# Kernel optimization log

Measured on AMD Instinct MI355X. Metric: run time of the kernel, lower is better.

Reference implementation:

```python
import jax, jax.numpy as jnp
import numpy as np

H = 16      # num_head
DH = 64     # d_head
D = H * DH  # d_model
NEG = -10000.0


def _proj(x, W, b):
    # torch Linear: y = x @ W^T + b
    return jnp.einsum('bld,od->blo', x, W) + b


def _heads(x):
    b, l, _ = x.shape
    return x.reshape(b, l, H, DH)


def _attn_logits(feat_q, mask_q, feat_k, mask_k, Wq, bq, Wk, bk):
    q = _heads(_proj(feat_q, Wq, bq))   # b lq h dh
    k = _heads(_proj(feat_k, Wk, bk))   # b lk h dh
    logits = jnp.einsum('bqhd,bkhd->bhqk', q, k)
    m = mask_q[:, None, :, None] & mask_k[:, None, None, :]  # b 1 lq lk
    return jnp.where(m, logits, NEG)


def setup_inputs() -> dict:
    key = jax.random.key(0)
    ks = jax.random.split(key, 12)
    B, Lv, Lt = 4, 1024, 256
    scale = 1.0 / np.sqrt(D).astype(np.float32)
    inp = {
        'vid_feat': jax.random.normal(ks[0], (B, Lv, D), jnp.float32),
        'vid_mask': jax.random.bernoulli(ks[1], 0.9, (B, Lv)),
        'txt_feat': jax.random.normal(ks[2], (B, Lt, D), jnp.float32),
        'txt_mask': jax.random.bernoulli(ks[3], 0.9, (B, Lt)),
    }
    names = ['v2v', 't2v', 'v2t', 't2t']
    for i, n in enumerate(names):
        inp['W_' + n] = jax.random.normal(ks[4 + i], (3, D, D), jnp.float32) * scale
        inp['b_' + n] = jax.random.normal(ks[8 + i], (3, D), jnp.float32) * 0.01
    return inp


def reference(vid_feat, vid_mask, txt_feat, txt_mask,
              W_v2v, b_v2v, W_t2v, b_t2v, W_v2t, b_v2t, W_t2t, b_t2t):
    B, Lv, _ = vid_feat.shape
    B, Lt, _ = txt_feat.shape
    # sr_ratio == 1: vid_feat_sr == vid_feat, vid_mask_sr == vid_mask
    vid_feat_sr, vid_mask_sr = vid_feat, vid_mask

    # values (proj index 2), concatenated along key length
    v_value = jnp.concatenate([_proj(vid_feat_sr, W_v2v[2], b_v2v[2]),
                               _proj(txt_feat, W_t2v[2], b_t2v[2])], axis=1)
    v_value = _heads(v_value)  # b (Lv+Lt) h dh
    t_value = jnp.concatenate([_proj(vid_feat_sr, W_v2t[2], b_v2t[2]),
                               _proj(txt_feat, W_t2t[2], b_t2t[2])], axis=1)
    t_value = _heads(t_value)

    v2v = _attn_logits(vid_feat, vid_mask, vid_feat_sr, vid_mask_sr,
                       W_v2v[0], b_v2v[0], W_v2v[1], b_v2v[1])
    t2v = _attn_logits(vid_feat, vid_mask, txt_feat, txt_mask,
                       W_t2v[0], b_t2v[0], W_t2v[1], b_t2v[1])
    v2t = _attn_logits(txt_feat, txt_mask, vid_feat_sr, vid_mask_sr,
                       W_v2t[0], b_v2t[0], W_v2t[1], b_v2t[1])
    t2t = _attn_logits(txt_feat, txt_mask, txt_feat, txt_mask,
                       W_t2t[0], b_t2t[0], W_t2t[1], b_t2t[1])

    v_logits = jnp.concatenate([v2v, t2v], axis=-1)  # b h Lv (Lv+Lt)
    t_logits = jnp.concatenate([v2t, t2t], axis=-1)  # b h Lt (Lv+Lt)
    inv_sqrt_dh = jnp.float32(1.0 / np.sqrt(DH))

    # NOTE: original applies softmax, THEN divides by sqrt(d_head) (faithful)
    vid_out = jnp.einsum('bhqk,bkhd->bqhd',
                         jax.nn.softmax(v_logits, axis=-1) * inv_sqrt_dh,
                         v_value).reshape(B, Lv, D)
    txt_out = jnp.einsum('bhqk,bkhd->bqhd',
                         jax.nn.softmax(t_logits, axis=-1) * inv_sqrt_dh,
                         t_value).reshape(B, Lt, D)
    return vid_out, txt_out
```

## Files before the change

### kernel.cpp

```cpp
#include <hip/hip_runtime.h>


typedef __attribute__((ext_vector_type(8))) _Float16  half8;
typedef __attribute__((ext_vector_type(4))) _Float16  half4;
typedef __attribute__((ext_vector_type(4))) float     f32x4;
typedef __attribute__((ext_vector_type(4))) unsigned int uint4v;
typedef __attribute__((ext_vector_type(2))) unsigned int uint2v;

#define MFMA_F16   __builtin_amdgcn_mfma_f32_16x16x32_f16
#define MFMA16_F16 __builtin_amdgcn_mfma_f32_16x16x16f16

#define LOG2E 1.4426950408889634f
#define NEGB  (-14426.950408889634f)

static __device__ __forceinline__ unsigned short f_to_f16u(float f) {
  _Float16 h = (_Float16)f;
  return __builtin_bit_cast(unsigned short, h);
}

#define GLOAD_LDS16(g, l)                                            \
  __builtin_amdgcn_global_load_lds(                                  \
      (const __attribute__((address_space(1))) void*)(g),            \
      (__attribute__((address_space(3))) void*)(l), 16, 0, 0)

struct CvtDesc { const float* src; unsigned short* dst; int n8; };
struct CvtArgs { CvtDesc d[14]; };

__global__ __launch_bounds__(256) void cvt_fp16(CvtArgs ca) {
  const CvtDesc dd = ca.d[blockIdx.y];
  const int n16 = dd.n8 >> 1;
  const int stride = gridDim.x * blockDim.x;
  for (int i = blockIdx.x * blockDim.x + threadIdx.x; i < n16; i += stride) {
    const f32x4* src = (const f32x4*)dd.src + (size_t)i * 4;
    const f32x4 a = src[0];
    const f32x4 b = src[1];
    const f32x4 c = src[2];
    const f32x4 d = src[3];
    half8 h0, h1;
    h0[0] = (_Float16)a[0]; h0[1] = (_Float16)a[1];
    h0[2] = (_Float16)a[2]; h0[3] = (_Float16)a[3];
    h0[4] = (_Float16)b[0]; h0[5] = (_Float16)b[1];
    h0[6] = (_Float16)b[2]; h0[7] = (_Float16)b[3];
    h1[0] = (_Float16)c[0]; h1[1] = (_Float16)c[1];
    h1[2] = (_Float16)c[2]; h1[3] = (_Float16)c[3];
    h1[4] = (_Float16)d[0]; h1[5] = (_Float16)d[1];
    h1[6] = (_Float16)d[2]; h1[7] = (_Float16)d[3];
    half8* dst = (half8*)dd.dst + (size_t)i * 2;
    dst[0] = h0;
    dst[1] = h1;
  }
}

static __device__ __forceinline__ void copy_out_tile(
    const unsigned short* Cs, unsigned short* dst, int tid,
    int b, int l0, int h0, int Ld, int soff, int mode) {
  for (int i = 0; i < 8; ++i) {
    const int c     = i * 256 + tid;
    const int major = c >> 4;
    const int kc    = c & 15;
    if (mode == 1) {
      const int base = (kc >> 2) * 32 + (kc & 3) * 4;
      const int sw   = major & 7;
      const int o1   = major * 128 + (((base >> 3) ^ sw) << 3) + (base & 7);
      const int b2   = base + 16;
      const int o2   = major * 128 + (((b2 >> 3) ^ sw) << 3) + (b2 & 7);
      const uint2v lo = *(const uint2v*)&Cs[o1];
      const uint2v hi = *(const uint2v*)&Cs[o2];
      uint4v val; val[0] = lo[0]; val[1] = lo[1]; val[2] = hi[0]; val[3] = hi[1];
      const int hh = h0 + (major >> 6);
      const int dh = major & 63;
      const int k  = soff + l0 + (kc >> 2) * 32;
      const size_t el = (size_t)(b * 16 + hh) * 81920 + (size_t)(k >> 5) * 2048 +
                        dh * 32 + (kc & 3) * 8;
      *(uint4v*)(dst + el) = val;
    } else {
      const uint4v val =
          *(const uint4v*)&Cs[major * 128 + ((kc ^ (major & 7)) << 3)];
      if (mode == 0) {
        const size_t el =
            ((size_t)(b * 16 + h0 + (kc >> 3)) * Ld + soff + l0 + major) * 64 +
            (kc & 7) * 8;
        *(uint4v*)(dst + el) = val;
      } else {
        const int k   = soff + l0 + major;
        const int dh0 = (kc & 7) * 8;
        const size_t el = (size_t)(b * 16 + h0 + (kc >> 3)) * 81920 +
                          (size_t)(k >> 4) * 1024 + (dh0 >> 5) * 512 +
                          (k & 15) * 32 + ((dh0 >> 3) & 3) * 8;
        *(uint4v*)(dst + el) = val;
      }
    }
  }
}

struct ProjDescH {
  const unsigned short* X;
  const unsigned short* W;
  const float* Bv;
  unsigned short* dst;
  int M, lxsh, Ld, soff, mode;
  float oscale;
};
struct ProjArgsH { ProjDescH d[12]; };

__global__ __launch_bounds__(256) void proj_gemm_h(ProjArgsH pa) {
  const ProjDescH dd = pa.d[blockIdx.z];
  const int m0 = blockIdx.y * 128;
  if (m0 >= dd.M) return;
  const int n0 = blockIdx.x * 128;

  __shared__ __align__(16) unsigned char smem[32768];
  unsigned short* As = (unsigned short*)smem;
  unsigned short* Bs = As + 4096;
  unsigned short* Cs = (unsigned short*)smem;

  const int tid  = threadIdx.x;
  const int lane = tid & 63;
  const int w    = tid >> 6;
  const int wr   = (w >> 1) * 64;
  const int wc   = (w & 1) * 64;
  const int ql   = lane & 15;
  const int qd   = lane >> 4;

  f32x4 acc[4][4];
  for (int i = 0; i < 4; ++i)
    for (int j = 0; j < 4; ++j) acc[i][j] = (f32x4)(0.0f);

  const unsigned short* Xg = dd.X + (size_t)m0 * 1024;
  const unsigned short* Wg = dd.W + (size_t)n0 * 1024;

  for (int k0 = 0; k0 < 1024; k0 += 32) {
    __syncthreads();
    for (int half = 0; half < 2; ++half) {
      const int cb  = w * 128 + half * 64;
      const int c   = cb + lane;
      const int row = c >> 2;
      const int kcg = (c & 3) ^ (row & 3);
      GLOAD_LDS16(Xg + row * 1024 + k0 + kcg * 8, As + cb * 8);
      GLOAD_LDS16(Wg + row * 1024 + k0 + kcg * 8, Bs + cb * 8);
    }
    __syncthreads();

    half8 af[4], bf[4];
    for (int mt = 0; mt < 4; ++mt) {
      const int row = wr + mt * 16 + ql;
      af[mt] = *(const half8*)&As[row * 32 + ((qd ^ (row & 3)) << 3)];
    }
    for (int nt = 0; nt < 4; ++nt) {
      const int row = wc + nt * 16 + ql;
      bf[nt] = *(const half8*)&Bs[row * 32 + ((qd ^ (row & 3)) << 3)];
    }
    for (int mt = 0; mt < 4; ++mt)
      for (int nt = 0; nt < 4; ++nt)
        acc[mt][nt] = MFMA_F16(af[mt], bf[nt], acc[mt][nt], 0, 0, 0);
  }

  float bv[4];
  for (int nt = 0; nt < 4; ++nt)
    bv[nt] = dd.Bv[n0 + wc + nt * 16 + ql];

  __syncthreads();

  for (int mt = 0; mt < 4; ++mt) {
    for (int nt = 0; nt < 4; ++nt) {
      const int nl = wc + nt * 16 + ql;
      for (int r = 0; r < 4; ++r) {
        const int ml = wr + mt * 16 + qd * 4 + r;
        const int row = dd.mode == 1 ? nl : ml;
        const int col = dd.mode == 1 ? ml : nl;
        const float v = (acc[mt][nt][r] + bv[nt]) * dd.oscale;
        Cs[row * 128 + (((col >> 3) ^ (row & 7)) << 3) + (col & 7)] = f_to_f16u(v);
      }
    }
  }
  __syncthreads();

  copy_out_tile(Cs, dd.dst, tid, m0 >> dd.lxsh, m0 & ((1 << dd.lxsh) - 1),
                n0 >> 6, dd.Ld, dd.soff, dd.mode);
}

struct ProjDesc {
  const float* X;
  const float* W;
  const float* Bv;
  unsigned short* dst;
  int M, lxsh, Ld, soff, mode;
  float oscale;
};
struct ProjArgs { ProjDesc d[12]; };

static __device__ __forceinline__ half8 cvt8sw(const float* base, int row, int g0) {
  const int sw = row & 7;
  const f32x4 a = *(const f32x4*)(base + (row * 8 + (g0 ^ sw)) * 4);
  const f32x4 b = *(const f32x4*)(base + (row * 8 + ((g0 + 1) ^ sw)) * 4);
  half8 h;
  h[0] = (_Float16)a[0]; h[1] = (_Float16)a[1];
  h[2] = (_Float16)a[2]; h[3] = (_Float16)a[3];
  h[4] = (_Float16)b[0]; h[5] = (_Float16)b[1];
  h[6] = (_Float16)b[2]; h[7] = (_Float16)b[3];
  return h;
}

__global__ __launch_bounds__(256) void proj_gemm_f32(ProjArgs pa) {
  const ProjDesc dd = pa.d[blockIdx.z];
  const int m0 = blockIdx.y * 128;
  if (m0 >= dd.M) return;
  const int n0 = blockIdx.x * 128;

  __shared__ __align__(16) unsigned char smem[32768];
  float* As = (float*)smem;
  float* Bs = As + 4096;
  unsigned short* Cs = (unsigned short*)smem;

  const int tid  = threadIdx.x;
  const int lane = tid & 63;
  const int w    = tid >> 6;
  const int wr   = (w >> 1) * 64;
  const int wc   = (w & 1) * 64;
  const int ql   = lane & 15;
  const int qd   = lane >> 4;

  f32x4 acc[4][4];
  for (int i = 0; i < 4; ++i)
    for (int j = 0; j < 4; ++j) acc[i][j] = (f32x4)(0.0f);

  const float* Xg = dd.X + (size_t)m0 * 1024;
  const float* Wg = dd.W + (size_t)n0 * 1024;

  for (int k0 = 0; k0 < 1024; k0 += 32) {
    __syncthreads();
    for (int j = 0; j < 4; ++j) {
      const int cb  = (j * 4 + w) * 64;
      const int c   = cb + lane;
      const int row = c >> 3;
      const int kcg = (c & 7) ^ (row & 7);
      GLOAD_LDS16(Xg + row * 1024 + k0 + kcg * 4, As + cb * 4);
      GLOAD_LDS16(Wg + row * 1024 + k0 + kcg * 4, Bs + cb * 4);
    }
    __syncthreads();

    half8 af[4], bf[4];
    for (int mt = 0; mt < 4; ++mt)
      af[mt] = cvt8sw(As, wr + mt * 16 + ql, qd * 2);
    for (int nt = 0; nt < 4; ++nt)
      bf[nt] = cvt8sw(Bs, wc + nt * 16 + ql, qd * 2);
    for (int mt = 0; mt < 4; ++mt)
      for (int nt = 0; nt < 4; ++nt)
        acc[mt][nt] = MFMA_F16(af[mt], bf[nt], acc[mt][nt], 0, 0, 0);
  }

  float bv[4];
  for (int nt = 0; nt < 4; ++nt)
    bv[nt] = dd.Bv[n0 + wc + nt * 16 + ql];

  __syncthreads();

  for (int mt = 0; mt < 4; ++mt) {
    for (int nt = 0; nt < 4; ++nt) {
      const int nl = wc + nt * 16 + ql;
      for (int r = 0; r < 4; ++r) {
        const int ml = wr + mt * 16 + qd * 4 + r;
        const int row = dd.mode == 1 ? nl : ml;
        const int col = dd.mode == 1 ? ml : nl;
        const float v = (acc[mt][nt][r] + bv[nt]) * dd.oscale;
        Cs[row * 128 + (((col >> 3) ^ (row & 7)) << 3) + (col & 7)] = f_to_f16u(v);
      }
    }
  }
  __syncthreads();

  copy_out_tile(Cs, dd.dst, tid, m0 >> dd.lxsh, m0 & ((1 << dd.lxsh) - 1),
                n0 >> 6, dd.Ld, dd.soff, dd.mode);
}

__global__ __launch_bounds__(256) void attn_flash7(
    const unsigned short* __restrict__ Qa_v, const unsigned short* __restrict__ Qb_v,
    const unsigned short* __restrict__ K_v,  const unsigned short* __restrict__ V_vT,
    const unsigned short* __restrict__ Qa_t, const unsigned short* __restrict__ Qb_t,
    const unsigned short* __restrict__ K_t,  const unsigned short* __restrict__ V_tT,
    const int* __restrict__ vmask, const int* __restrict__ tmask,
    float* __restrict__ out_v, float* __restrict__ out_t) {
  __shared__ __align__(16) unsigned short KVs[8192];
  __shared__ __align__(16) float kb_s[1280];

  const int bid = blockIdx.x;
  const int sid = (bid & 7) * 160 + (bid >> 3);
  const int bh  = sid / 20;
  const int sub = sid - bh * 20;

  const bool vside = sub < 16;
  const int  Lq    = vside ? 1024 : 256;
  const int  qblk  = vside ? sub : sub - 16;
  const unsigned short* Qa = vside ? Qa_v : Qa_t;
  const unsigned short* Qb = vside ? Qb_v : Qb_t;
  const unsigned short* K  = vside ? K_v  : K_t;
  const unsigned short* VT = vside ? V_vT : V_tT;
  const int* mq  = vside ? vmask : tmask;
  float*     out = vside ? out_v : out_t;

  const int b = bh >> 4;
  const int h = bh & 15;
  const int tid  = threadIdx.x;
  const int w    = tid >> 6;
  const int lane = tid & 63;
  const int ql = lane & 15, qd = lane >> 4;
  const int q0 = qblk * 64 + w * 16;

  const unsigned short* Kb = K  + (size_t)bh * 81920;
  const unsigned short* Vb = VT + (size_t)bh * 81920;

  {
    const int* kmv = vmask + b * 1024;
    const int* kmt = tmask + b * 256;
    for (int i = tid; i < 1280; i += 256) {
      const int mk = (i < 1024) ? kmv[i] : kmt[i - 1024];
      kb_s[i] = mk ? 0.0f : NEGB;
    }
  }

  const int gsw  = (tid ^ ((tid >> 3) & 3)) * 8;
  const int wlds = w * 512;

#define STAGE6(nb, k0s)                                                     \
  do {                                                                      \
    const unsigned short* Kt_ = Kb + (size_t)((k0s) >> 4) * 1024;           \
    const unsigned short* Vt_ = Vb + (size_t)((k0s) >> 5) * 2048;           \
    unsigned short* Ld_ = KVs + (nb) * 4096 + wlds;                         \
    GLOAD_LDS16(Kt_ + gsw, Ld_);                                            \
    GLOAD_LDS16(Vt_ + gsw, Ld_ + 2048);                                     \
  } while (0)

  STAGE6(0, 0);

  const unsigned short* Qab = Qa + ((size_t)bh * Lq + q0) * 64;
  const unsigned short* Qbb = Qb + ((size_t)bh * Lq + q0) * 64;
  half8 aA[2], aB[2];
  for (int ks = 0; ks < 2; ++ks) {
    aA[ks] = *(const half8*)&Qab[ql * 64 + ks * 32 + qd * 8];
    aB[ks] = *(const half8*)&Qbb[ql * 64 + ks * 32 + qd * 8];
  }
  const int mqs = mq[b * Lq + q0 + ql];

  const int swc = (qd ^ ((ql >> 1) & 3)) * 8;

  float m = -1e30f, l = 0.0f;
  f32x4 o[4];
  for (int nt = 0; nt < 4; ++nt) o[nt] = (f32x4)(0.0f);

  int cur = 0;
#define TILE7(tt, QF)                                                       \
  {                                                                         \
    __syncthreads();                    \
    if ((tt) < 39) STAGE6(cur ^ 1, ((tt) + 1) * 32);                        \
    const unsigned short* Ls = KVs + cur * 4096;                            \
    half8 vv[4];                                                            \
    for (int nt = 0; nt < 4; ++nt)                                          \
      vv[nt] = *(const half8*)&Ls[2048 + (nt * 16 + ql) * 32 + swc];        \
    f32x4 sv[2];                                                            \
    for (int s = 0; s < 2; ++s) {                                           \
      f32x4 S = *(const f32x4*)&kb_s[(tt) * 32 + s * 16 + qd * 4];          \
      const unsigned short* Kt = Ls + s * 1024;                             \
      const half8 kf0 = *(const half8*)&Kt[ql * 32 + swc];                  \
      const half8 kf1 = *(const half8*)&Kt[512 + ql * 32 + swc];            \
      S = MFMA_F16(kf0, QF[0], S, 0, 0, 0);                                 \
      S = MFMA_F16(kf1, QF[1], S, 0, 0, 0);                                 \
      for (int r = 0; r < 4; ++r) sv[s][r] = mqs ? S[r] : NEGB;             \
    }                                                                       \
    const float t0 = fmaxf(fmaxf(sv[0][0], sv[0][1]), sv[0][2]);            \
    const float t1 = fmaxf(fmaxf(sv[0][3], sv[1][0]), sv[1][1]);            \
    const float t2 = fmaxf(fmaxf(sv[1][2], sv[1][3]), t0);                  \
    float bm = fmaxf(t1, t2);                                               \
    bm = fmaxf(bm, __shfl_xor(bm, 16, 64));                                 \
    bm = fmaxf(bm, __shfl_xor(bm, 32, 64));                                 \
    if (__any(bm > m)) {                        \
      const float nm = fmaxf(m, bm);                                        \
      const float alpha = __builtin_amdgcn_exp2f(m - nm);                   \
      l *= alpha;                                                           \
      for (int nt = 0; nt < 4; ++nt)                                        \
        for (int r = 0; r < 4; ++r) o[nt][r] *= alpha;                      \
      m = nm;                                                               \
    }                                                                       \
    half4 pv[2];                                                            \
    float lsum = 0.0f;                                                      \
    for (int s = 0; s < 2; ++s)                                             \
      for (int r = 0; r < 4; ++r) {                                         \
        const float p = __builtin_amdgcn_exp2f(sv[s][r] - m);               \
        lsum += p;                                                          \
        pv[s][r] = (_Float16)p;                                             \
      }                                                                     \
    l += lsum;                                                              \
    for (int nt = 0; nt < 4; ++nt) {                                        \
      const half4 vlo = __builtin_shufflevector(vv[nt], vv[nt], 0, 1, 2, 3);\
      const half4 vhi = __builtin_shufflevector(vv[nt], vv[nt], 4, 5, 6, 7);\
      o[nt] = MFMA16_F16(vlo, pv[0], o[nt], 0, 0, 0);                       \
      o[nt] = MFMA16_F16(vhi, pv[1], o[nt], 0, 0, 0);                       \
    }                                                                       \
    cur ^= 1;                                                               \
  }

  for (int t = 0; t < 32; ++t) TILE7(t, aA);
  for (int t = 32; t < 40; ++t) TILE7(t, aB);
#undef TILE7
#undef STAGE6

  l += __shfl_xor(l, 16, 64);
  l += __shfl_xor(l, 32, 64);
  const float inv = 0.125f / l;

  float* ob = out + ((size_t)(b * Lq + q0 + ql)) * 1024 + h * 64;
  for (int nt = 0; nt < 4; ++nt) {
    f32x4 r;
    for (int j = 0; j < 4; ++j) r[j] = o[nt][j] * inv;
    *(f32x4*)(ob + nt * 16 + qd * 4) = r;
  }
}

extern "C" void kernel_launch(void* const* d_in, const int* in_sizes, int n_in,
                              void* d_out, int out_size, void* d_ws, size_t ws_size,
                              hipStream_t stream) {
  const float* vid   = (const float*)d_in[0];
  const int*   vmask = (const int*)d_in[1];
  const float* txt   = (const float*)d_in[2];
  const int*   tmask = (const int*)d_in[3];
  const float* Wsrc[4] = {(const float*)d_in[4], (const float*)d_in[6],
                          (const float*)d_in[8], (const float*)d_in[10]};
  const float* Bsrc[4] = {(const float*)d_in[5], (const float*)d_in[7],
                          (const float*)d_in[9], (const float*)d_in[11]};

  const int DD = 1024 * 1024, Dm = 1024, MEG = 1048576;

  unsigned short* ws = (unsigned short*)d_ws;
  unsigned short* Qa_v = ws;
  unsigned short* Qb_v = ws + 4194304;
  unsigned short* K_v  = ws + 8388608;
  unsigned short* V_vT = ws + 13631488;
  unsigned short* Qa_t = ws + 18874368;
  unsigned short* Qb_t = ws + 19922944;
  unsigned short* K_t  = ws + 20971520;
  unsigned short* V_tT = ws + 26214400;
  unsigned short* Xv_h = ws + 31457280;
  unsigned short* Xt_h = ws + 35651584;
  unsigned short* Wh   = ws + 36700160;

  const size_t need = (size_t)49283072 * 2;
  const bool use_h = ws_size >= need;

  if (use_h) {
    CvtArgs ca;
    ca.d[0] = CvtDesc{vid, Xv_h, 4194304 / 8};
    ca.d[1] = CvtDesc{txt, Xt_h, 1048576 / 8};
    for (int s = 0; s < 4; ++s)
      for (int j = 0; j < 3; ++j)
        ca.d[2 + s * 3 + j] = CvtDesc{Wsrc[s] + j * DD, Wh + (s * 3 + j) * MEG, DD / 8};
    cvt_fp16<<<dim3(256, 14), dim3(256), 0, stream>>>(ca);

    ProjArgsH pa;
    auto set = [&](int i, const unsigned short* X, int wi, const float* Bv,
                   unsigned short* dst, int M, int lxsh, int Ld, int soff, int mode,
                   float osc) {
      pa.d[i] = ProjDescH{X, Wh + wi * MEG, Bv, dst, M, lxsh, Ld, soff, mode, osc};
    };
    set(0,  Xv_h, 0,  Bsrc[0],          Qa_v, 4096, 10, 1024, 0,    0, LOG2E);
    set(1,  Xv_h, 1,  Bsrc[0] + Dm,     K_v,  4096, 10, 1280, 0,    2, 1.0f);
    set(2,  Xv_h, 2,  Bsrc[0] + 2 * Dm, V_vT, 4096, 10, 1280, 0,    1, 1.0f);
    set(3,  Xv_h, 3,  Bsrc[1],          Qb_v, 4096, 10, 1024, 0,    0, LOG2E);
    set(4,  Xt_h, 4,  Bsrc[1] + Dm,     K_v,  1024, 8,  1280, 1024, 2, 1.0f);
    set(5,  Xt_h, 5,  Bsrc[1] + 2 * Dm, V_vT, 1024, 8,  1280, 1024, 1, 1.0f);
    set(6,  Xt_h, 6,  Bsrc[2],          Qa_t, 1024, 8,  256,  0,    0, LOG2E);
    set(7,  Xv_h, 7,  Bsrc[2] + Dm,     K_t,  4096, 10, 1280, 0,    2, 1.0f);
    set(8,  Xv_h, 8,  Bsrc[2] + 2 * Dm, V_tT, 4096, 10, 1280, 0,    1, 1.0f);
    set(9,  Xt_h, 9,  Bsrc[3],          Qb_t, 1024, 8,  256,  0,    0, LOG2E);
    set(10, Xt_h, 10, Bsrc[3] + Dm,     K_t,  1024, 8,  1280, 1024, 2, 1.0f);
    set(11, Xt_h, 11, Bsrc[3] + 2 * Dm, V_tT, 1024, 8,  1280, 1024, 1, 1.0f);

    proj_gemm_h<<<dim3(8, 32, 12), dim3(256), 0, stream>>>(pa);
  } else {
    ProjArgs pa;
    auto set = [&](int i, const float* X, const float* W, const float* Bv,
                   unsigned short* dst, int M, int lxsh, int Ld, int soff, int mode,
                   float osc) {
      pa.d[i] = ProjDesc{X, W, Bv, dst, M, lxsh, Ld, soff, mode, osc};
    };
    set(0,  vid, Wsrc[0],          Bsrc[0],          Qa_v, 4096, 10, 1024, 0,    0, LOG2E);
    set(1,  vid, Wsrc[0] + DD,     Bsrc[0] + Dm,     K_v,  4096, 10, 1280, 0,    2, 1.0f);
    set(2,  vid, Wsrc[0] + 2 * DD, Bsrc[0] + 2 * Dm, V_vT, 4096, 10, 1280, 0,    1, 1.0f);
    set(3,  vid, Wsrc[1],          Bsrc[1],          Qb_v, 4096, 10, 1024, 0,    0, LOG2E);
    set(4,  txt, Wsrc[1] + DD,     Bsrc[1] + Dm,     K_v,  1024, 8,  1280, 1024, 2, 1.0f);
    set(5,  txt, Wsrc[1] + 2 * DD, Bsrc[1] + 2 * Dm, V_vT, 1024, 8,  1280, 1024, 1, 1.0f);
    set(6,  txt, Wsrc[2],          Bsrc[2],          Qa_t, 1024, 8,  256,  0,    0, LOG2E);
    set(7,  vid, Wsrc[2] + DD,     Bsrc[2] + Dm,     K_t,  4096, 10, 1280, 0,    2, 1.0f);
    set(8,  vid, Wsrc[2] + 2 * DD, Bsrc[2] + 2 * Dm, V_tT, 4096, 10, 1280, 0,    1, 1.0f);
    set(9,  txt, Wsrc[3],          Bsrc[3],          Qb_t, 1024, 8,  256,  0,    0, LOG2E);
    set(10, txt, Wsrc[3] + DD,     Bsrc[3] + Dm,     K_t,  1024, 8,  1280, 1024, 2, 1.0f);
    set(11, txt, Wsrc[3] + 2 * DD, Bsrc[3] + 2 * Dm, V_tT, 1024, 8,  1280, 1024, 1, 1.0f);

    proj_gemm_f32<<<dim3(8, 32, 12), dim3(256), 0, stream>>>(pa);
  }

  float* out_v = (float*)d_out;
  float* out_t = out_v + 4 * 1024 * 1024;
  attn_flash7<<<dim3(1280), dim3(256), 0, stream>>>(
      Qa_v, Qb_v, K_v, V_vT, Qa_t, Qb_t, K_t, V_tT,
      vmask, tmask, out_v, out_t);
}
```

Measured before the change: 286.1 us.

## Double-buffer projection GEMM LDS tiles with async prefetch of next k-slice

The projection GEMM now uses two LDS buffers, each holding an A and a B tile. It issues the global-to-LDS loads for the next 32-wide k slice before computing on the current one, and waits with vmcnt(4) so that only the older loads must be complete. The goal is to hide global load latency behind the MFMA work instead of stalling on every iteration. This depends on the 32KB of shared memory fitting two buffers and on hand-placed waitcnt and barrier ordering being correct.

Measured after the change: 299.2 us. 1.05x slower.

```diff
diff --git a/kernel.cpp b/kernel.cpp
--- a/kernel.cpp
+++ b/kernel.cpp
@@ -110,8 +110,7 @@
   const int n0 = blockIdx.x * 128;
 
   __shared__ __align__(16) unsigned char smem[32768];
-  unsigned short* As = (unsigned short*)smem;
-  unsigned short* Bs = As + 4096;
+  unsigned short* AB = (unsigned short*)smem;
   unsigned short* Cs = (unsigned short*)smem;
 
   const int tid  = threadIdx.x;
@@ -129,18 +128,34 @@
   const unsigned short* Xg = dd.X + (size_t)m0 * 1024;
   const unsigned short* Wg = dd.W + (size_t)n0 * 1024;
 
-  for (int k0 = 0; k0 < 1024; k0 += 32) {
-    __syncthreads();
-    for (int half = 0; half < 2; ++half) {
-      const int cb  = w * 128 + half * 64;
-      const int c   = cb + lane;
-      const int row = c >> 2;
-      const int kcg = (c & 3) ^ (row & 3);
-      GLOAD_LDS16(Xg + row * 1024 + k0 + kcg * 8, As + cb * 8);
-      GLOAD_LDS16(Wg + row * 1024 + k0 + kcg * 8, Bs + cb * 8);
-    }
-    __syncthreads();
-
+#define STAGEP(nb, k0s)                                                      \
+  do {                                                                       \
+    unsigned short* As_ = AB + (nb) * 8192;                                  \
+    for (int half_ = 0; half_ < 2; ++half_) {                                \
+      const int cb_  = w * 128 + half_ * 64;                                 \
+      const int c_   = cb_ + lane;                                           \
+      const int row_ = c_ >> 2;                                              \
+      const int kcg_ = (c_ & 3) ^ (row_ & 3);                                \
+      GLOAD_LDS16(Xg + row_ * 1024 + (k0s) + kcg_ * 8, As_ + cb_ * 8);       \
+      GLOAD_LDS16(Wg + row_ * 1024 + (k0s) + kcg_ * 8, As_ + 4096 + cb_ * 8);\
+    }                                                                        \
+  } while (0)
+
+  STAGEP(0, 0);
+
+  for (int t = 0; t < 32; ++t) {
+    __builtin_amdgcn_s_barrier();
+    if (t < 31) {
+      STAGEP((t + 1) & 1, (t + 1) * 32);
+      asm volatile("s_waitcnt vmcnt(4)" ::: "memory");
+    } else {
+      asm volatile("s_waitcnt vmcnt(0)" ::: "memory");
+    }
+    __builtin_amdgcn_sched_barrier(0);
+    __builtin_amdgcn_s_barrier();
+
+    const unsigned short* As = AB + (t & 1) * 8192;
+    const unsigned short* Bs = As + 4096;
     half8 af[4], bf[4];
     for (int mt = 0; mt < 4; ++mt) {
       const int row = wr + mt * 16 + ql;
@@ -154,6 +169,7 @@
       for (int nt = 0; nt < 4; ++nt)
         acc[mt][nt] = MFMA_F16(af[mt], bf[nt], acc[mt][nt], 0, 0, 0);
   }
+#undef STAGEP
 
   float bv[4];
   for (int nt = 0; nt < 4; ++nt)
```

## Enlarge f16 projection GEMM tile to 256x128 with 512-thread blocks

Applied to the files above, without the earlier changes.

The half-precision projection GEMM now uses 512-thread blocks covering 256 rows by 128 columns, so each weight tile loaded into LDS is shared by twice as many rows and the grid is halved. The epilogue stages the two 128-row halves through shared memory one after the other, and copy_out_tile takes a thread count so it works with either block size. The change targets redundant weight loads and per-block overhead, at the cost of fewer blocks for the GPU to schedule and extra barriers in the epilogue.

After: 286.9 us. No clear change (+0.3%).

```diff
diff --git a/kernel.cpp b/kernel.cpp
--- a/kernel.cpp
+++ b/kernel.cpp
@@ -52,10 +52,9 @@
 }
 
 static __device__ __forceinline__ void copy_out_tile(
-    const unsigned short* Cs, unsigned short* dst, int tid,
+    const unsigned short* Cs, unsigned short* dst, int tid, int nthr,
     int b, int l0, int h0, int Ld, int soff, int mode) {
-  for (int i = 0; i < 8; ++i) {
-    const int c     = i * 256 + tid;
+  for (int c = tid; c < 2048; c += nthr) {
     const int major = c >> 4;
     const int kc    = c & 15;
     if (mode == 1) {
@@ -103,15 +102,124 @@
 };
 struct ProjArgsH { ProjDescH d[12]; };
 
-__global__ __launch_bounds__(256) void proj_gemm_h(ProjArgsH pa) {
+__global__ __launch_bounds__(512) void proj_gemm_h(ProjArgsH pa) {
   const ProjDescH dd = pa.d[blockIdx.z];
+  const int m0 = blockIdx.y * 256;
+  if (m0 >= dd.M) return;
+  const int n0 = blockIdx.x * 128;
+
+  __shared__ __align__(16) unsigned char smem[32768];
+  unsigned short* As = (unsigned short*)smem;
+  unsigned short* Bs = As + 8192;
+  unsigned short* Cs = (unsigned short*)smem;
+
+  const int tid  = threadIdx.x;
+  const int lane = tid & 63;
+  const int w    = tid >> 6;
+  const int wrF  = (w >> 1) * 64;
+  const int wc   = (w & 1) * 64;
+  const int ql   = lane & 15;
+  const int qd   = lane >> 4;
+
+  f32x4 acc[4][4];
+  for (int i = 0; i < 4; ++i)
+    for (int j = 0; j < 4; ++j) acc[i][j] = (f32x4)(0.0f);
+
+  const unsigned short* Xg = dd.X + (size_t)m0 * 1024;
+  const unsigned short* Wg = dd.W + (size_t)n0 * 1024;
+
+  for (int k0 = 0; k0 < 1024; k0 += 32) {
+    __syncthreads();
+    {
+      const int cb0 = w * 64;
+      const int c0  = cb0 + lane;
+      const int r0  = c0 >> 2;
+      GLOAD_LDS16(Xg + r0 * 1024 + k0 + ((c0 & 3) ^ (r0 & 3)) * 8, As + cb0 * 8);
+      const int cb1 = 512 + w * 64;
+      const int c1  = cb1 + lane;
+      const int r1  = c1 >> 2;
+      GLOAD_LDS16(Xg + r1 * 1024 + k0 + ((c1 & 3) ^ (r1 & 3)) * 8, As + cb1 * 8);
+      const int cb2 = w * 64;
+      const int c2  = cb2 + lane;
+      const int r2  = c2 >> 2;
+      GLOAD_LDS16(Wg + r2 * 1024 + k0 + ((c2 & 3) ^ (r2 & 3)) * 8, Bs + cb2 * 8);
+    }
+    __syncthreads();
+
+    half8 af[4], bf[4];
+    for (int mt = 0; mt < 4; ++mt) {
+      const int row = wrF + mt * 16 + ql;
+      af[mt] = *(const half8*)&As[row * 32 + ((qd ^ (row & 3)) << 3)];
+    }
+    for (int nt = 0; nt < 4; ++nt) {
+      const int row = wc + nt * 16 + ql;
+      bf[nt] = *(const half8*)&Bs[row * 32 + ((qd ^ (row & 3)) << 3)];
+    }
+    for (int mt = 0; mt < 4; ++mt)
+      for (int nt = 0; nt < 4; ++nt)
+        acc[mt][nt] = MFMA_F16(af[mt], bf[nt], acc[mt][nt], 0, 0, 0);
+  }
+
+  float bv[4];
+  for (int nt = 0; nt < 4; ++nt)
+    bv[nt] = dd.Bv[n0 + wc + nt * 16 + ql];
+
+  for (int rh = 0; rh < 2; ++rh) {
+    __syncthreads();
+    if ((w >> 2) == rh) {
+      const int wrL = ((w >> 1) & 1) * 64;
+      for (int mt = 0; mt < 4; ++mt) {
+        for (int nt = 0; nt < 4; ++nt) {
+          const int nl = wc + nt * 16 + ql;
+          for (int r = 0; r < 4; ++r) {
+            const int ml = wrL + mt * 16 + qd * 4 + r;
+            const int row = dd.mode == 1 ? nl : ml;
+            const int col = dd.mode == 1 ? ml : nl;
+            const float v = (acc[mt][nt][r] + bv[nt]) * dd.oscale;
+            Cs[row * 128 + (((col >> 3) ^ (row & 7)) << 3) + (col & 7)] =
+                f_to_f16u(v);
+          }
+        }
+      }
+    }
+    __syncthreads();
+    const int m0p = m0 + rh * 128;
+    copy_out_tile(Cs, dd.dst, tid, 512, m0p >> dd.lxsh,
+                  m0p & ((1 << dd.lxsh) - 1), n0 >> 6, dd.Ld, dd.soff, dd.mode);
+  }
+}
+
+struct ProjDesc {
+  const float* X;
+  const float* W;
+  const float* Bv;
+  unsigned short* dst;
+  int M, lxsh, Ld, soff, mode;
+  float oscale;
+};
+struct ProjArgs { ProjDesc d[12]; };
+
+static __device__ __forceinline__ half8 cvt8sw(const float* base, int row, int g0) {
+  const int sw = row & 7;
+  const f32x4 a = *(const f32x4*)(base + (row * 8 + (g0 ^ sw)) * 4);
+  const f32x4 b = *(const f32x4*)(base + (row * 8 + ((g0 + 1) ^ sw)) * 4);
+  half8 h;
+  h[0] = (_Float16)a[0]; h[1] = (_Float16)a[1];
+  h[2] = (_Float16)a[2]; h[3] = (_Float16)a[3];
+  h[4] = (_Float16)b[0]; h[5] = (_Float16)b[1];
+  h[6] = (_Float16)b[2]; h[7] = (_Float16)b[3];
+  return h;
+}
+
+__global__ __launch_bounds__(256) void proj_gemm_f32(ProjArgs pa) {
+  const ProjDesc dd = pa.d[blockIdx.z];
   const int m0 = blockIdx.y * 128;
   if (m0 >= dd.M) return;
   const int n0 = blockIdx.x * 128;
 
   __shared__ __align__(16) unsigned char smem[32768];
-  unsigned short* As = (unsigned short*)smem;
-  unsigned short* Bs = As + 4096;
+  float* As = (float*)smem;
+  float* Bs = As + 4096;
   unsigned short* Cs = (unsigned short*)smem;
 
   const int tid  = threadIdx.x;
@@ -126,30 +234,26 @@
   for (int i = 0; i < 4; ++i)
     for (int j = 0; j < 4; ++j) acc[i][j] = (f32x4)(0.0f);
 
-  const unsigned short* Xg = dd.X + (size_t)m0 * 1024;
-  const unsigned short* Wg = dd.W + (size_t)n0 * 1024;
+  const float* Xg = dd.X + (size_t)m0 * 1024;
+  const float* Wg = dd.W + (size_t)n0 * 1024;
 
   for (int k0 = 0; k0 < 1024; k0 += 32) {
     __syncthreads();
-    for (int half = 0; half < 2; ++half) {
-      const int cb  = w * 128 + half * 64;
+    for (int j = 0; j < 4; ++j) {
+      const int cb  = (j * 4 + w) * 64;
       const int c   = cb + lane;
-      const int row = c >> 2;
-      const int kcg = (c & 3) ^ (row & 3);
-      GLOAD_LDS16(Xg + row * 1024 + k0 + kcg * 8, As + cb * 8);
-      GLOAD_LDS16(Wg + row * 1024 + k0 + kcg * 8, Bs + cb * 8);
+      const int row = c >> 3;
+      const int kcg = (c & 7) ^ (row & 7);
+      GLOAD_LDS16(Xg + row * 1024 + k0 + kcg * 4, As + cb * 4);
+      GLOAD_LDS16(Wg + row * 1024 + k0 + kcg * 4, Bs + cb * 4);
     }
     __syncthreads();
 
     half8 af[4], bf[4];
-    for (int mt = 0; mt < 4; ++mt) {
-      const int row = wr + mt * 16 + ql;
-      af[mt] = *(const half8*)&As[row * 32 + ((qd ^ (row & 3)) << 3)];
-    }
-    for (int nt = 0; nt < 4; ++nt) {
-      const int row = wc + nt * 16 + ql;
-      bf[nt] = *(const half8*)&Bs[row * 32 + ((qd ^ (row & 3)) << 3)];
-    }
+    for (int mt = 0; mt < 4; ++mt)
+      af[mt] = cvt8sw(As, wr + mt * 16 + ql, qd * 2);
+    for (int nt = 0; nt < 4; ++nt)
+      bf[nt] = cvt8sw(Bs, wc + nt * 16 + ql, qd * 2);
     for (int mt = 0; mt < 4; ++mt)
       for (int nt = 0; nt < 4; ++nt)
         acc[mt][nt] = MFMA_F16(af[mt], bf[nt], acc[mt][nt], 0, 0, 0);
@@ -175,101 +279,7 @@
   }
   __syncthreads();
 
-  copy_out_tile(Cs, dd.dst, tid, m0 >> dd.lxsh, m0 & ((1 << dd.lxsh) - 1),
-                n0 >> 6, dd.Ld, dd.soff, dd.mode);
-}
-
-struct ProjDesc {
-  const float* X;
-  const float* W;
-  const float* Bv;
-  unsigned short* dst;
-  int M, lxsh, Ld, soff, mode;
-  float oscale;
-};
-struct ProjArgs { ProjDesc d[12]; };
-
-static __device__ __forceinline__ half8 cvt8sw(const float* base, int row, int g0) {
-  const int sw = row & 7;
-  const f32x4 a = *(const f32x4*)(base + (row * 8 + (g0 ^ sw)) * 4);
-  const f32x4 b = *(const f32x4*)(base + (row * 8 + ((g0 + 1) ^ sw)) * 4);
-  half8 h;
-  h[0] = (_Float16)a[0]; h[1] = (_Float16)a[1];
-  h[2] = (_Float16)a[2]; h[3] = (_Float16)a[3];
-  h[4] = (_Float16)b[0]; h[5] = (_Float16)b[1];
-  h[6] = (_Float16)b[2]; h[7] = (_Float16)b[3];
-  return h;
-}
-
-__global__ __launch_bounds__(256) void proj_gemm_f32(ProjArgs pa) {
-  const ProjDesc dd = pa.d[blockIdx.z];
-  const int m0 = blockIdx.y * 128;
-  if (m0 >= dd.M) return;
-  const int n0 = blockIdx.x * 128;
-
-  __shared__ __align__(16) unsigned char smem[32768];
-  float* As = (float*)smem;
-  float* Bs = As + 4096;
-  unsigned short* Cs = (unsigned short*)smem;
-
-  const int tid  = threadIdx.x;
-  const int lane = tid & 63;
-  const int w    = tid >> 6;
-  const int wr   = (w >> 1) * 64;
-  const int wc   = (w & 1) * 64;
-  const int ql   = lane & 15;
-  const int qd   = lane >> 4;
-
-  f32x4 acc[4][4];
-  for (int i = 0; i < 4; ++i)
-    for (int j = 0; j < 4; ++j) acc[i][j] = (f32x4)(0.0f);
-
-  const float* Xg = dd.X + (size_t)m0 * 1024;
-  const float* Wg = dd.W + (size_t)n0 * 1024;
-
-  for (int k0 = 0; k0 < 1024; k0 += 32) {
-    __syncthreads();
-    for (int j = 0; j < 4; ++j) {
-      const int cb  = (j * 4 + w) * 64;
-      const int c   = cb + lane;
-      const int row = c >> 3;
-      const int kcg = (c & 7) ^ (row & 7);
-      GLOAD_LDS16(Xg + row * 1024 + k0 + kcg * 4, As + cb * 4);
-      GLOAD_LDS16(Wg + row * 1024 + k0 + kcg * 4, Bs + cb * 4);
-    }
-    __syncthreads();
-
-    half8 af[4], bf[4];
-    for (int mt = 0; mt < 4; ++mt)
-      af[mt] = cvt8sw(As, wr + mt * 16 + ql, qd * 2);
-    for (int nt = 0; nt < 4; ++nt)
-      bf[nt] = cvt8sw(Bs, wc + nt * 16 + ql, qd * 2);
-    for (int mt = 0; mt < 4; ++mt)
-      for (int nt = 0; nt < 4; ++nt)
-        acc[mt][nt] = MFMA_F16(af[mt], bf[nt], acc[mt][nt], 0, 0, 0);
-  }
-
-  float bv[4];
-  for (int nt = 0; nt < 4; ++nt)
-    bv[nt] = dd.Bv[n0 + wc + nt * 16 + ql];
-
-  __syncthreads();
-
-  for (int mt = 0; mt < 4; ++mt) {
-    for (int nt = 0; nt < 4; ++nt) {
-      const int nl = wc + nt * 16 + ql;
-      for (int r = 0; r < 4; ++r) {
-        const int ml = wr + mt * 16 + qd * 4 + r;
-        const int row = dd.mode == 1 ? nl : ml;
-        const int col = dd.mode == 1 ? ml : nl;
-        const float v = (acc[mt][nt][r] + bv[nt]) * dd.oscale;
-        Cs[row * 128 + (((col >> 3) ^ (row & 7)) << 3) + (col & 7)] = f_to_f16u(v);
-      }
-    }
-  }
-  __syncthreads();
-
-  copy_out_tile(Cs, dd.dst, tid, m0 >> dd.lxsh, m0 & ((1 << dd.lxsh) - 1),
+  copy_out_tile(Cs, dd.dst, tid, 256, m0 >> dd.lxsh, m0 & ((1 << dd.lxsh) - 1),
                 n0 >> 6, dd.Ld, dd.soff, dd.mode);
 }
 
@@ -473,7 +483,7 @@
     set(10, Xt_h, 10, Bsrc[3] + Dm,     K_t,  1024, 8,  1280, 1024, 2, 1.0f);
     set(11, Xt_h, 11, Bsrc[3] + 2 * Dm, V_tT, 1024, 8,  1280, 1024, 1, 1.0f);
 
-    proj_gemm_h<<<dim3(8, 32, 12), dim3(256), 0, stream>>>(pa);
+    proj_gemm_h<<<dim3(8, 16, 12), dim3(512), 0, stream>>>(pa);
   } else {
     ProjArgs pa;
     auto set = [&](int i, const float* X, const float* W, const float* Bv,
```
